# Kernel tuning notes

Measured on AMD Instinct MI355X. Metric: run time of the kernel, lower is better.

## Reference

```python
import jax, jax.numpy as jnp
import numpy as np

DIM = 256
N = 262144
LN_EPS = 1e-5


def setup_inputs() -> dict:
    key = jax.random.key(0)
    ks = jax.random.split(key, 16)
    d = DIM
    inp = {
        "x": jax.random.normal(ks[0], (N, d), dtype=jnp.float32),
        # main cell params (torch Linear stores weight as [out, in])
        "W_slow": jax.random.normal(ks[1], (d, d), dtype=jnp.float32) / np.sqrt(d),
        "V_slow": jax.random.normal(ks[2], (d, d), dtype=jnp.float32) * (0.1 / np.sqrt(d)),
        "gate_w": jax.random.normal(ks[3], (1, d), dtype=jnp.float32) / np.sqrt(d),
        "gate_b": jnp.zeros((1,), dtype=jnp.float32),
        # homeostatic core: Linear(4,16) -> LN(16) -> Tanh -> Linear(16,8) -> ReLU -> Linear(8,4) -> Sigmoid
        "sens1_w": jax.random.normal(ks[4], (16, 4), dtype=jnp.float32) * 0.5,
        "sens1_b": jnp.zeros((16,), dtype=jnp.float32),
        "ln_g": jnp.ones((16,), dtype=jnp.float32),
        "ln_b": jnp.zeros((16,), dtype=jnp.float32),
        "sens2_w": jax.random.normal(ks[5], (8, 16), dtype=jnp.float32) * 0.25,
        "sens2_b": jnp.zeros((8,), dtype=jnp.float32),
        "act_w": jax.random.normal(ks[6], (4, 8), dtype=jnp.float32) * 0.35,
        "act_b": jnp.zeros((4,), dtype=jnp.float32),
        # persistent Hebbian memory buffer
        "semantic_memory": jax.random.normal(ks[7], (d, d), dtype=jnp.float32) * 0.01,
    }
    return inp


def _homeostatic_controls(x, h_raw, w_norm, sens1_w, sens1_b, ln_g, ln_b,
                          sens2_w, sens2_b, act_w, act_b):
    # state vector: [surprise, excitation, fatigue, coherence]  -> [N, 4]
    surprise = jnp.abs(jnp.var(x, axis=1) - 0.5)          # unbiased=False variance
    excitation = jnp.mean(jnp.abs(h_raw), axis=1)
    fatigue = jnp.full_like(surprise, w_norm)
    coherence = jnp.full_like(surprise, 0.5)              # loss_val is None
    state = jnp.stack([surprise, excitation, fatigue, coherence], axis=1)
    z = state @ sens1_w.T + sens1_b                        # [N,16]
    mu = jnp.mean(z, axis=-1, keepdims=True)
    var = jnp.mean((z - mu) ** 2, axis=-1, keepdims=True)
    z = (z - mu) * jax.lax.rsqrt(var + LN_EPS) * ln_g + ln_b
    z = jnp.tanh(z)
    z = jax.nn.relu(z @ sens2_w.T + sens2_b)               # [N,8]
    controls = jax.nn.sigmoid(z @ act_w.T + act_b)         # [N,4]
    return controls


def reference(x, W_slow, V_slow, gate_w, gate_b,
              sens1_w, sens1_b, ln_g, ln_b, sens2_w, sens2_b, act_w, act_b,
              semantic_memory):
    # v = clamp(V_slow(x), -2, 2)
    v = jnp.clip(x @ V_slow.T, -2.0, 2.0)                  # [N, d]

    # homeostatic core (no_grad in torch)
    h_raw = x @ W_slow.T
    w_norm = jnp.linalg.norm(W_slow)
    controls = _homeostatic_controls(x, h_raw, w_norm, sens1_w, sens1_b,
                                     ln_g, ln_b, sens2_w, sens2_b, act_w, act_b)
    metabolic_rate = jnp.mean(controls[:, 0])
    gate_value = jnp.mean(controls[:, 2])

    gate = jax.nn.sigmoid(v @ gate_w.T + gate_b) * gate_value  # [N,1]
    output = jnp.clip(gate * v, -2.0, 2.0)

    # training-mode Hebbian memory update (no_grad in torch)
    batch = x.shape[0]
    hebb = (v.T @ x) / batch                               # [d, d]
    forget = jnp.mean(v ** 2, axis=0)[:, None] * semantic_memory
    delta = jnp.tanh(hebb - forget)
    mem = semantic_memory + delta * metabolic_rate * 0.1
    mem_norm = jnp.maximum(jnp.linalg.norm(mem), 1e-6)
    new_memory = mem / mem_norm * 0.5

    return output, new_memory
```

## Files before the change

### kernel.cpp

```cpp
#include <hip/hip_runtime.h>
#include <hip/hip_bf16.h>


#define NTOK 262144

typedef short s16x8 __attribute__((ext_vector_type(8)));
typedef float f32x4 __attribute__((ext_vector_type(4)));
typedef unsigned int u32x4 __attribute__((ext_vector_type(4)));
typedef __bf16 bf16x8 __attribute__((ext_vector_type(8)));

static __device__ __forceinline__ float b2f(short s) {
  unsigned int u = ((unsigned int)(unsigned short)s) << 16;
  return __builtin_bit_cast(float, u);
}
static __device__ __forceinline__ short f2b(float f) {
  __hip_bfloat16 h = __float2bfloat16(f);
  return (short)__builtin_bit_cast(unsigned short, h);
}
static __device__ __forceinline__ float clip2(float f) {
  return fminf(2.f, fmaxf(-2.f, f));
}
static __device__ __forceinline__ unsigned int packu(short lo, short hi) {
  return (unsigned int)(unsigned short)lo | ((unsigned int)(unsigned short)hi << 16);
}
static __device__ __forceinline__ f32x4 mfma16(s16x8 a, s16x8 b, f32x4 c) {
  return __builtin_amdgcn_mfma_f32_16x16x32_bf16(
      __builtin_bit_cast(bf16x8, a), __builtin_bit_cast(bf16x8, b), c, 0, 0, 0);
}

__global__ __launch_bounds__(1024) void k_prep(const float* __restrict__ W,
                                               float* __restrict__ scal,
                                               float* __restrict__ colv2) {
  int tid = threadIdx.x;
  if (tid >= 1 && tid <= 3) scal[tid] = 0.f;
  if (tid < 256) colv2[tid] = 0.f;
  float s = 0.f;
#pragma unroll
  for (int p = 0; p < 16; ++p) {
    f32x4 w4 = *(const f32x4*)(W + (size_t)(p * 1024 + tid) * 4);
#pragma unroll
    for (int e = 0; e < 4; ++e) s += w4[e] * w4[e];
  }
#pragma unroll
  for (int d = 1; d < 64; d <<= 1) s += __shfl_xor(s, d);
  __shared__ float r[16];
  if ((tid & 63) == 0) r[tid >> 6] = s;
  __syncthreads();
  if (tid == 0) {
    float t = 0.f;
#pragma unroll
    for (int i = 0; i < 16; ++i) t += r[i];
    scal[0] = t;
  }
}

__global__ __launch_bounds__(512, 2) void k_main(
    const float* __restrict__ x, const float* __restrict__ Wm,
    const float* __restrict__ Vm, const float* __restrict__ gw,
    const float* __restrict__ gb, const float* __restrict__ s1w,
    const float* __restrict__ s1b, const float* __restrict__ lng,
    const float* __restrict__ lnb, const float* __restrict__ s2w,
    const float* __restrict__ s2b, const float* __restrict__ aw,
    const float* __restrict__ ab, short* __restrict__ v_out,
    float* __restrict__ g_out, float* __restrict__ scal) {
  __shared__ __align__(16) short lds[128 * 40 + 2 * 256 * 40];
  short* xs = lds;
  short* vs = lds + 128 * 40;
  short* ws2 = vs + 256 * 40;
  int tid = threadIdx.x;
  int lane = tid & 63, wid = tid >> 6;
  int lr = lane & 15, lg = lane >> 4;
  int wr = wid >> 2, wc = wid & 3;
  size_t r0 = (size_t)blockIdx.x * 128;

  f32x4 accv[4][4] = {};
  f32x4 acch[4][4] = {};
  float sx = 0.f, sxx = 0.f;
  int srow = tid >> 2, ssub = tid & 3;

  for (int ks = 0; ks < 8; ++ks) {
    int k0 = ks * 32;
    {
      int row = tid >> 2, kc = tid & 3;
      const float* src = x + (r0 + row) * 256 + k0 + kc * 8;
      f32x4 a0 = *(const f32x4*)(src);
      f32x4 a1 = *(const f32x4*)(src + 4);
      s16x8 c;
#pragma unroll
      for (int e = 0; e < 4; ++e) { c[e] = f2b(a0[e]); c[4 + e] = f2b(a1[e]); }
      *(s16x8*)(xs + row * 40 + kc * 8) = c;
    }
#pragma unroll
    for (int p = 0; p < 2; ++p) {
      int cidx = p * 512 + tid;
      int row = cidx >> 2, kc = cidx & 3;
      const float* src = Vm + (size_t)row * 256 + k0 + kc * 8;
      f32x4 a0 = *(const f32x4*)(src);
      f32x4 a1 = *(const f32x4*)(src + 4);
      s16x8 c;
#pragma unroll
      for (int e = 0; e < 4; ++e) { c[e] = f2b(a0[e]); c[4 + e] = f2b(a1[e]); }
      *(s16x8*)(vs + row * 40 + kc * 8) = c;
    }
#pragma unroll
    for (int p = 0; p < 2; ++p) {
      int cidx = p * 512 + tid;
      int row = cidx >> 2, kc = cidx & 3;
      const float* src = Wm + (size_t)row * 256 + k0 + kc * 8;
      f32x4 a0 = *(const f32x4*)(src);
      f32x4 a1 = *(const f32x4*)(src + 4);
      s16x8 c;
#pragma unroll
      for (int e = 0; e < 4; ++e) { c[e] = f2b(a0[e]); c[4 + e] = f2b(a1[e]); }
      *(s16x8*)(ws2 + row * 40 + kc * 8) = c;
    }
    __syncthreads();
    {
      s16x8 xa = *(const s16x8*)(xs + srow * 40 + ssub * 8);
#pragma unroll
      for (int e = 0; e < 8; ++e) { float f = b2f(xa[e]); sx += f; sxx += f * f; }
    }
    s16x8 bv[4], bw[4];
#pragma unroll
    for (int nf = 0; nf < 4; ++nf) {
      bv[nf] = *(const s16x8*)(vs + (wc * 64 + nf * 16 + lr) * 40 + lg * 8);
      bw[nf] = *(const s16x8*)(ws2 + (wc * 64 + nf * 16 + lr) * 40 + lg * 8);
    }
#pragma unroll
    for (int mf = 0; mf < 4; ++mf) {
      s16x8 a = *(const s16x8*)(xs + (wr * 64 + mf * 16 + lr) * 40 + lg * 8);
#pragma unroll
      for (int nf = 0; nf < 4; ++nf) {
        accv[mf][nf] = mfma16(a, bv[nf], accv[mf][nf]);
        acch[mf][nf] = mfma16(a, bw[nf], acch[mf][nf]);
      }
    }
    __syncthreads();
  }

  float gw4[4];
#pragma unroll
  for (int nf = 0; nf < 4; ++nf) gw4[nf] = gw[wc * 64 + nf * 16 + lr];
  float gd[4][4], hb[4][4];
#pragma unroll
  for (int mf = 0; mf < 4; ++mf)
#pragma unroll
    for (int e = 0; e < 4; ++e) { gd[mf][e] = 0.f; hb[mf][e] = 0.f; }
#pragma unroll
  for (int mf = 0; mf < 4; ++mf)
#pragma unroll
    for (int nf = 0; nf < 4; ++nf)
#pragma unroll
      for (int e = 0; e < 4; ++e) {
        float v = clip2(accv[mf][nf][e]);
        accv[mf][nf][e] = v;
        gd[mf][e] += v * gw4[nf];
        hb[mf][e] += fabsf(acch[mf][nf][e]);
      }
#pragma unroll
  for (int d = 1; d < 16; d <<= 1)
#pragma unroll
    for (int mf = 0; mf < 4; ++mf)
#pragma unroll
      for (int e = 0; e < 4; ++e) {
        gd[mf][e] += __shfl_xor(gd[mf][e], d);
        hb[mf][e] += __shfl_xor(hb[mf][e], d);
      }
  sx += __shfl_xor(sx, 1); sx += __shfl_xor(sx, 2);
  sxx += __shfl_xor(sxx, 1); sxx += __shfl_xor(sxx, 2);

  __syncthreads();
  float* red = (float*)lds;
  if (tid < 256) red[tid] = 0.f;
  __syncthreads();
  if (lr == 0) {
#pragma unroll
    for (int mf = 0; mf < 4; ++mf)
#pragma unroll
      for (int e = 0; e < 4; ++e) {
        int row = wr * 64 + mf * 16 + lg * 4 + e;
        atomicAdd(&red[row], gd[mf][e]);
        atomicAdd(&red[128 + row], hb[mf][e]);
      }
  }
  if (ssub == 0) { red[256 + srow] = sx; red[384 + srow] = sxx; }
#pragma unroll
  for (int mf = 0; mf < 4; ++mf)
#pragma unroll
    for (int nf = 0; nf < 4; ++nf)
#pragma unroll
      for (int e = 0; e < 4; ++e) {
        int row = wr * 64 + mf * 16 + lg * 4 + e;
        int col = wc * 64 + nf * 16 + lr;
        v_out[(r0 + row) * 256 + col] = f2b(accv[mf][nf][e]);
      }
  __syncthreads();

  float c0v = 0.f, c2v = 0.f;
  if (tid < 128) {
    int row = tid;
    float mean = red[256 + row] * (1.f / 256.f);
    float var = red[384 + row] * (1.f / 256.f) - mean * mean;
    float st[4];
    st[0] = fabsf(var - 0.5f);
    st[1] = red[128 + row] * (1.f / 256.f);
    st[2] = sqrtf(scal[0]);
    st[3] = 0.5f;
    float z[16];
#pragma unroll
    for (int o = 0; o < 16; ++o) {
      float a = s1b[o];
#pragma unroll
      for (int i = 0; i < 4; ++i) a += s1w[o * 4 + i] * st[i];
      z[o] = a;
    }
    float mu = 0.f;
#pragma unroll
    for (int o = 0; o < 16; ++o) mu += z[o];
    mu *= (1.f / 16.f);
    float vz = 0.f;
#pragma unroll
    for (int o = 0; o < 16; ++o) { float d2 = z[o] - mu; vz += d2 * d2; }
    vz *= (1.f / 16.f);
    float rs = rsqrtf(vz + 1e-5f);
#pragma unroll
    for (int o = 0; o < 16; ++o)
      z[o] = tanhf((z[o] - mu) * rs * lng[o] + lnb[o]);
    float z2[8];
#pragma unroll
    for (int o = 0; o < 8; ++o) {
      float a = s2b[o];
#pragma unroll
      for (int i = 0; i < 16; ++i) a += s2w[o * 16 + i] * z[i];
      z2[o] = fmaxf(a, 0.f);
    }
    float cc[2];
#pragma unroll
    for (int q = 0; q < 2; ++q) {
      int o = q * 2;
      float a = ab[o];
#pragma unroll
      for (int i = 0; i < 8; ++i) a += aw[o * 8 + i] * z2[i];
      cc[q] = 1.f / (1.f + expf(-a));
    }
    c0v = cc[0]; c2v = cc[1];
    float graw = red[row] + gb[0];
    g_out[r0 + row] = 1.f / (1.f + expf(-graw));
  }
#pragma unroll
  for (int d = 1; d < 64; d <<= 1) {
    c0v += __shfl_xor(c0v, d);
    c2v += __shfl_xor(c2v, d);
  }
  if (lane == 0 && wid < 2) {
    atomicAdd(&scal[1], c0v);
    atomicAdd(&scal[2], c2v);
  }
}

__global__ __launch_bounds__(512, 2) void k_hebb(
    const float* __restrict__ x, const short* __restrict__ v_in,
    const float* __restrict__ g_sig, const float* __restrict__ scal,
    float* __restrict__ colv2, float* __restrict__ parts,
    float* __restrict__ out0) {
  __shared__ __align__(16) unsigned int ldsT[2 * 256 * 17];
  unsigned int* vT = ldsT;
  unsigned int* xT = ldsT + 256 * 17;
  int tid = threadIdx.x;
  int lane = tid & 63, wid = tid >> 6;
  int lr = lane & 15, lg = lane >> 4;
  int wr = wid >> 2, wc = wid & 3;
  size_t n0 = (size_t)blockIdx.x * 1024;
  float gv = scal[2] * (1.f / 262144.f);

  f32x4 acc[8][4] = {};
  float cv2[8] = {0.f, 0.f, 0.f, 0.f, 0.f, 0.f, 0.f, 0.f};
  int np = tid >> 5, ic = tid & 31, i0 = ic * 8;

  for (int nt = 0; nt < 32; ++nt) {
    size_t nr = n0 + nt * 32 + np * 2;
    s16x8 va = *(const s16x8*)(v_in + nr * 256 + i0);
    s16x8 vb = *(const s16x8*)(v_in + (nr + 1) * 256 + i0);
    f32x4 xa0 = *(const f32x4*)(x + nr * 256 + i0);
    f32x4 xa1 = *(const f32x4*)(x + nr * 256 + i0 + 4);
    f32x4 xb0 = *(const f32x4*)(x + (nr + 1) * 256 + i0);
    f32x4 xb1 = *(const f32x4*)(x + (nr + 1) * 256 + i0 + 4);
    float sa = g_sig[nr] * gv, sb = g_sig[nr + 1] * gv;
    f32x4 oa0, oa1, ob0, ob1;
#pragma unroll
    for (int j = 0; j < 4; ++j) {
      float fa = b2f(va[j]), fA = b2f(va[4 + j]);
      float fb = b2f(vb[j]), fB = b2f(vb[4 + j]);
      cv2[j] += fa * fa + fb * fb;
      cv2[4 + j] += fA * fA + fB * fB;
      oa0[j] = clip2(fa * sa); oa1[j] = clip2(fA * sa);
      ob0[j] = clip2(fb * sb); ob1[j] = clip2(fB * sb);
      vT[(i0 + j) * 17 + np] = packu(va[j], vb[j]);
      vT[(i0 + 4 + j) * 17 + np] = packu(va[4 + j], vb[4 + j]);
      xT[(i0 + j) * 17 + np] = packu(f2b(xa0[j]), f2b(xb0[j]));
      xT[(i0 + 4 + j) * 17 + np] = packu(f2b(xa1[j]), f2b(xb1[j]));
    }
    *(f32x4*)(out0 + nr * 256 + i0) = oa0;
    *(f32x4*)(out0 + nr * 256 + i0 + 4) = oa1;
    *(f32x4*)(out0 + (nr + 1) * 256 + i0) = ob0;
    *(f32x4*)(out0 + (nr + 1) * 256 + i0 + 4) = ob1;
    __syncthreads();
    int npb = lg * 4;
    s16x8 bfr[4];
#pragma unroll
    for (int nf = 0; nf < 4; ++nf) {
      int j = wc * 64 + nf * 16 + lr;
      u32x4 q;
      q[0] = xT[j * 17 + npb]; q[1] = xT[j * 17 + npb + 1];
      q[2] = xT[j * 17 + npb + 2]; q[3] = xT[j * 17 + npb + 3];
      bfr[nf] = __builtin_bit_cast(s16x8, q);
    }
#pragma unroll
    for (int mf = 0; mf < 8; ++mf) {
      int i = wr * 128 + mf * 16 + lr;
      u32x4 q;
      q[0] = vT[i * 17 + npb]; q[1] = vT[i * 17 + npb + 1];
      q[2] = vT[i * 17 + npb + 2]; q[3] = vT[i * 17 + npb + 3];
      s16x8 afr = __builtin_bit_cast(s16x8, q);
#pragma unroll
      for (int nf = 0; nf < 4; ++nf)
        acc[mf][nf] = mfma16(afr, bfr[nf], acc[mf][nf]);
    }
    __syncthreads();
  }
  float* myp = parts + (size_t)blockIdx.x * 65536;
#pragma unroll
  for (int mf = 0; mf < 8; ++mf)
#pragma unroll
    for (int nf = 0; nf < 4; ++nf)
#pragma unroll
      for (int e = 0; e < 4; ++e) {
        int i = wr * 128 + mf * 16 + lg * 4 + e;
        int j = wc * 64 + nf * 16 + lr;
        myp[i * 256 + j] = acc[mf][nf][e];
      }
  __syncthreads();
  float* cred = (float*)ldsT;
  if (tid < 256) cred[tid] = 0.f;
  __syncthreads();
#pragma unroll
  for (int j = 0; j < 8; ++j) atomicAdd(&cred[i0 + j], cv2[j]);
  __syncthreads();
  if (tid < 256) atomicAdd(&colv2[tid], cred[tid]);
}

__global__ __launch_bounds__(256) void k_mem1(
    const float* __restrict__ parts, const float* __restrict__ colv2,
    const float* __restrict__ sm, float* __restrict__ mem,
    float* __restrict__ scal) {
  int i = blockIdx.x, j = threadIdx.x;
  float hebb = 0.f;
#pragma unroll 8
  for (int p = 0; p < 256; ++p) hebb += parts[(size_t)p * 65536 + i * 256 + j];
  hebb *= (1.f / 262144.f);
  float mr = scal[1] * (1.f / 262144.f);
  float smv = sm[i * 256 + j];
  float forget = colv2[i] * (1.f / 262144.f) * smv;
  float delta = tanhf(hebb - forget);
  float m = smv + delta * mr * 0.1f;
  mem[i * 256 + j] = m;
  float s = m * m;
#pragma unroll
  for (int d = 1; d < 64; d <<= 1) s += __shfl_xor(s, d);
  __shared__ float r4[4];
  if ((j & 63) == 0) r4[j >> 6] = s;
  __syncthreads();
  if (j == 0) atomicAdd(&scal[3], r4[0] + r4[1] + r4[2] + r4[3]);
}

__global__ __launch_bounds__(256) void k_mem2(const float* __restrict__ mem,
                                              const float* __restrict__ scal,
                                              float* __restrict__ out1) {
  int idx = blockIdx.x * 256 + threadIdx.x;
  float scale = 0.5f / fmaxf(sqrtf(scal[3]), 1e-6f);
  out1[idx] = mem[idx] * scale;
}

extern "C" void kernel_launch(void* const* d_in, const int* in_sizes, int n_in,
                              void* d_out, int out_size, void* d_ws, size_t ws_size,
                              hipStream_t stream) {
  (void)in_sizes; (void)n_in; (void)out_size; (void)ws_size;
  const float* x   = (const float*)d_in[0];
  const float* Wm  = (const float*)d_in[1];
  const float* Vm  = (const float*)d_in[2];
  const float* gw  = (const float*)d_in[3];
  const float* gb  = (const float*)d_in[4];
  const float* s1w = (const float*)d_in[5];
  const float* s1b = (const float*)d_in[6];
  const float* lng = (const float*)d_in[7];
  const float* lnb = (const float*)d_in[8];
  const float* s2w = (const float*)d_in[9];
  const float* s2b = (const float*)d_in[10];
  const float* aw  = (const float*)d_in[11];
  const float* ab  = (const float*)d_in[12];
  const float* sm  = (const float*)d_in[13];
  float* out0 = (float*)d_out;
  float* out1 = out0 + (size_t)NTOK * 256;

  char* w = (char*)d_ws;
  short* v_ws  = (short*)w;
  float* g_ws  = (float*)(w + 134217728);
  float* scal  = (float*)(w + 135266304);
  float* colv2 = (float*)(w + 135266560);
  float* mem   = (float*)(w + 135267584);
  float* parts = (float*)(w + 135529728);

  k_prep<<<1, 1024, 0, stream>>>(Wm, scal, colv2);
  k_main<<<2048, 512, 0, stream>>>(x, Wm, Vm, gw, gb, s1w, s1b, lng, lnb,
                                   s2w, s2b, aw, ab, v_ws, g_ws, scal);
  k_hebb<<<256, 512, 0, stream>>>(x, v_ws, g_ws, scal, colv2, parts, out0);
  k_mem1<<<256, 256, 0, stream>>>(parts, colv2, sm, mem, scal);
  k_mem2<<<256, 256, 0, stream>>>(mem, scal, out1);
}
```

Baseline: 420.9 us.

## Pre-convert weights to bf16 and register-prefetch next K-slice in main GEMM

k_prep now converts V_slow and W_slow to bf16 once across 16 blocks and accumulates the Frobenius norm atomically; a memset replaces the in-kernel zeroing of scal/colv2. k_main loads the pre-converted bf16 weights directly, prefetches the next K-slice of x and weights into registers while MFMAs run, and computes row sum and sum-of-squares from fp32 x instead of re-reading LDS. The goal is to remove redundant per-block fp32 weight conversion and hide global load latency. Launch bounds move to 4 waves per EU, which may pressure registers given the large accumulator arrays. The stats are now computed from fp32 rather than bf16-rounded x, a small numeric change.

```diff
diff --git a/kernel.cpp b/kernel.cpp
--- a/kernel.cpp
+++ b/kernel.cpp
@@ -4,6 +4,7 @@
 
 #define NTOK 262144
 
+typedef short s16x4 __attribute__((ext_vector_type(4)));
 typedef short s16x8 __attribute__((ext_vector_type(8)));
 typedef float f32x4 __attribute__((ext_vector_type(4)));
 typedef unsigned int u32x4 __attribute__((ext_vector_type(4)));
@@ -28,35 +29,40 @@
       __builtin_bit_cast(bf16x8, a), __builtin_bit_cast(bf16x8, b), c, 0, 0, 0);
 }
 
-__global__ __launch_bounds__(1024) void k_prep(const float* __restrict__ W,
-                                               float* __restrict__ scal,
-                                               float* __restrict__ colv2) {
-  int tid = threadIdx.x;
-  if (tid >= 1 && tid <= 3) scal[tid] = 0.f;
-  if (tid < 256) colv2[tid] = 0.f;
+__global__ __launch_bounds__(1024) void k_prep(const float* __restrict__ V,
+                                               const float* __restrict__ W,
+                                               short* __restrict__ Vb,
+                                               short* __restrict__ Wb,
+                                               float* __restrict__ scal) {
+  int t = blockIdx.x * 1024 + threadIdx.x;
+  f32x4 v4 = *(const f32x4*)(V + (size_t)t * 4);
+  f32x4 w4 = *(const f32x4*)(W + (size_t)t * 4);
+  s16x4 vb, wb;
   float s = 0.f;
 #pragma unroll
-  for (int p = 0; p < 16; ++p) {
-    f32x4 w4 = *(const f32x4*)(W + (size_t)(p * 1024 + tid) * 4);
-#pragma unroll
-    for (int e = 0; e < 4; ++e) s += w4[e] * w4[e];
-  }
+  for (int e = 0; e < 4; ++e) {
+    vb[e] = f2b(v4[e]);
+    wb[e] = f2b(w4[e]);
+    s += w4[e] * w4[e];
+  }
+  *(s16x4*)(Vb + (size_t)t * 4) = vb;
+  *(s16x4*)(Wb + (size_t)t * 4) = wb;
 #pragma unroll
   for (int d = 1; d < 64; d <<= 1) s += __shfl_xor(s, d);
   __shared__ float r[16];
-  if ((tid & 63) == 0) r[tid >> 6] = s;
-  __syncthreads();
-  if (tid == 0) {
-    float t = 0.f;
-#pragma unroll
-    for (int i = 0; i < 16; ++i) t += r[i];
-    scal[0] = t;
-  }
-}
-
-__global__ __launch_bounds__(512, 2) void k_main(
-    const float* __restrict__ x, const float* __restrict__ Wm,
-    const float* __restrict__ Vm, const float* __restrict__ gw,
+  if ((threadIdx.x & 63) == 0) r[threadIdx.x >> 6] = s;
+  __syncthreads();
+  if (threadIdx.x == 0) {
+    float tt = 0.f;
+#pragma unroll
+    for (int i = 0; i < 16; ++i) tt += r[i];
+    atomicAdd(&scal[0], tt);
+  }
+}
+
+__global__ __launch_bounds__(512, 4) void k_main(
+    const float* __restrict__ x, const short* __restrict__ Vb,
+    const short* __restrict__ Wb, const float* __restrict__ gw,
     const float* __restrict__ gb, const float* __restrict__ s1w,
     const float* __restrict__ s1b, const float* __restrict__ lng,
     const float* __restrict__ lnb, const float* __restrict__ s2w,
@@ -76,49 +82,51 @@
   f32x4 accv[4][4] = {};
   f32x4 acch[4][4] = {};
   float sx = 0.f, sxx = 0.f;
-  int srow = tid >> 2, ssub = tid & 3;
+
+  int srow = tid >> 2, skc = tid & 3;
+  int vrow0 = tid >> 2, vkc0 = tid & 3;
+  int vrow1 = 128 + (tid >> 2), vkc1 = tid & 3;
+
+  f32x4 rxa, rxb;
+  s16x8 rv0, rv1, rw0, rw1;
+
+  {
+    const float* src = x + (r0 + srow) * 256 + skc * 8;
+    rxa = *(const f32x4*)(src);
+    rxb = *(const f32x4*)(src + 4);
+    rv0 = *(const s16x8*)(Vb + (size_t)vrow0 * 256 + vkc0 * 8);
+    rv1 = *(const s16x8*)(Vb + (size_t)vrow1 * 256 + vkc1 * 8);
+    rw0 = *(const s16x8*)(Wb + (size_t)vrow0 * 256 + vkc0 * 8);
+    rw1 = *(const s16x8*)(Wb + (size_t)vrow1 * 256 + vkc1 * 8);
+  }
 
   for (int ks = 0; ks < 8; ++ks) {
-    int k0 = ks * 32;
     {
-      int row = tid >> 2, kc = tid & 3;
-      const float* src = x + (r0 + row) * 256 + k0 + kc * 8;
-      f32x4 a0 = *(const f32x4*)(src);
-      f32x4 a1 = *(const f32x4*)(src + 4);
       s16x8 c;
 #pragma unroll
-      for (int e = 0; e < 4; ++e) { c[e] = f2b(a0[e]); c[4 + e] = f2b(a1[e]); }
-      *(s16x8*)(xs + row * 40 + kc * 8) = c;
-    }
-#pragma unroll
-    for (int p = 0; p < 2; ++p) {
-      int cidx = p * 512 + tid;
-      int row = cidx >> 2, kc = cidx & 3;
-      const float* src = Vm + (size_t)row * 256 + k0 + kc * 8;
-      f32x4 a0 = *(const f32x4*)(src);
-      f32x4 a1 = *(const f32x4*)(src + 4);
-      s16x8 c;
-#pragma unroll
-      for (int e = 0; e < 4; ++e) { c[e] = f2b(a0[e]); c[4 + e] = f2b(a1[e]); }
-      *(s16x8*)(vs + row * 40 + kc * 8) = c;
-    }
-#pragma unroll
-    for (int p = 0; p < 2; ++p) {
-      int cidx = p * 512 + tid;
-      int row = cidx >> 2, kc = cidx & 3;
-      const float* src = Wm + (size_t)row * 256 + k0 + kc * 8;
-      f32x4 a0 = *(const f32x4*)(src);
-      f32x4 a1 = *(const f32x4*)(src + 4);
-      s16x8 c;
-#pragma unroll
-      for (int e = 0; e < 4; ++e) { c[e] = f2b(a0[e]); c[4 + e] = f2b(a1[e]); }
-      *(s16x8*)(ws2 + row * 40 + kc * 8) = c;
+      for (int e = 0; e < 4; ++e) {
+        float f0 = rxa[e], f1 = rxb[e];
+        sx += f0 + f1;
+        sxx += f0 * f0 + f1 * f1;
+        c[e] = f2b(f0);
+        c[4 + e] = f2b(f1);
+      }
+      *(s16x8*)(xs + srow * 40 + skc * 8) = c;
+      *(s16x8*)(vs + vrow0 * 40 + vkc0 * 8) = rv0;
+      *(s16x8*)(vs + vrow1 * 40 + vkc1 * 8) = rv1;
+      *(s16x8*)(ws2 + vrow0 * 40 + vkc0 * 8) = rw0;
+      *(s16x8*)(ws2 + vrow1 * 40 + vkc1 * 8) = rw1;
     }
     __syncthreads();
-    {
-      s16x8 xa = *(const s16x8*)(xs + srow * 40 + ssub * 8);
-#pragma unroll
-      for (int e = 0; e < 8; ++e) { float f = b2f(xa[e]); sx += f; sxx += f * f; }
+    if (ks < 7) {
+      int k0 = (ks + 1) * 32;
+      const float* src = x + (r0 + srow) * 256 + k0 + skc * 8;
+      rxa = *(const f32x4*)(src);
+      rxb = *(const f32x4*)(src + 4);
+      rv0 = *(const s16x8*)(Vb + (size_t)vrow0 * 256 + k0 + vkc0 * 8);
+      rv1 = *(const s16x8*)(Vb + (size_t)vrow1 * 256 + k0 + vkc1 * 8);
+      rw0 = *(const s16x8*)(Wb + (size_t)vrow0 * 256 + k0 + vkc0 * 8);
+      rw1 = *(const s16x8*)(Wb + (size_t)vrow1 * 256 + k0 + vkc1 * 8);
     }
     s16x8 bv[4], bw[4];
 #pragma unroll
@@ -183,7 +191,7 @@
         atomicAdd(&red[128 + row], hb[mf][e]);
       }
   }
-  if (ssub == 0) { red[256 + srow] = sx; red[384 + srow] = sxx; }
+  if (skc == 0) { red[256 + srow] = sx; red[384 + srow] = sxx; }
 #pragma unroll
   for (int mf = 0; mf < 4; ++mf)
 #pragma unroll
@@ -409,9 +417,12 @@
   float* colv2 = (float*)(w + 135266560);
   float* mem   = (float*)(w + 135267584);
   float* parts = (float*)(w + 135529728);
-
-  k_prep<<<1, 1024, 0, stream>>>(Wm, scal, colv2);
-  k_main<<<2048, 512, 0, stream>>>(x, Wm, Vm, gw, gb, s1w, s1b, lng, lnb,
+  short* Vb    = (short*)(w + 202638592);
+  short* Wb    = (short*)(w + 202769664);
+
+  hipMemsetAsync(scal, 0, 1280, stream);
+  k_prep<<<16, 1024, 0, stream>>>(Vm, Wm, Vb, Wb, scal);
+  k_main<<<2048, 512, 0, stream>>>(x, Vb, Wb, gw, gb, s1w, s1b, lng, lnb,
                                    s2w, s2b, aw, ab, v_ws, g_ws, scal);
   k_hebb<<<256, 512, 0, stream>>>(x, v_ws, g_ws, scal, colv2, parts, out0);
   k_mem1<<<256, 256, 0, stream>>>(parts, colv2, sm, mem, scal);
```

Result: slower. 1.267 ms (+201.1%).
